# Performance work log

Hardware: AMD Instinct MI355X
Metric: run time of the kernel (lower is better)

## Reference

```python
import jax, jax.numpy as jnp
import numpy as np
import math

C_IN, C_OUT = 256, 256
KH, KW = 3, 3
STRIDE, PAD = 1, 1
CURV = 1.0
SQRT_C = math.sqrt(CURV)
EPS = 1e-15

def _beta(a, b):
    return math.exp(math.lgamma(a) + math.lgamma(b) - math.lgamma(a + b))

BETA_NI = _beta(C_IN / 2.0, 0.5)                 # beta(n_i/2, 1/2)
BETA_N = _beta(C_IN * KH * KW / 2.0, 0.5)        # beta(n/2, 1/2)


def logmap0(y, axis):
    n = jnp.maximum(jnp.linalg.norm(y, axis=axis, keepdims=True), EPS)
    return jnp.arctanh(jnp.minimum(SQRT_C * n, 1.0 - 1e-7)) * y / (SQRT_C * n)


def expmap0(v, axis):
    n = jnp.maximum(jnp.linalg.norm(v, axis=axis, keepdims=True), EPS)
    return jnp.tanh(SQRT_C * n) * v / (SQRT_C * n)


def unfold(x):
    # torch.nn.Unfold: x [B,C,H,W] -> [B, C*KH*KW, L], channel-major patch order
    B, C, H, W = x.shape
    Ho = (H + 2 * PAD - KH) // STRIDE + 1
    Wo = (W + 2 * PAD - KW) // STRIDE + 1
    xp = jnp.pad(x, ((0, 0), (0, 0), (PAD, PAD), (PAD, PAD)))
    cols = [xp[:, :, i:i + STRIDE * Ho:STRIDE, j:j + STRIDE * Wo:STRIDE]
            for i in range(KH) for j in range(KW)]
    patches = jnp.stack(cols, axis=2)            # [B, C, KH*KW, Ho, Wo]
    return patches.reshape(B, C * KH * KW, Ho * Wo), Ho, Wo


def poincare_fc(x, z, r):
    # x: [..., D_in] on ball, z: [D_in, D_out], r: [D_out]
    x2 = jnp.sum(x * x, axis=-1, keepdims=True)
    lam = 2.0 / (1.0 - CURV * x2)                # conformal factor lambda_x
    z_norm = jnp.maximum(jnp.linalg.norm(z, axis=0), EPS)  # [D_out]
    xz = x @ z                                   # [..., D_out]
    two_csr = 2.0 * SQRT_C * r
    inner = (SQRT_C * lam * xz / z_norm * jnp.cosh(two_csr)
             - (lam - 1.0) * jnp.sinh(two_csr))
    v = 2.0 * z_norm / SQRT_C * jnp.arcsinh(inner)   # hyperplane distances
    w = jnp.sinh(SQRT_C * v) / SQRT_C
    return w / (1.0 + jnp.sqrt(1.0 + CURV * jnp.sum(w * w, axis=-1, keepdims=True)))


def setup_inputs() -> dict:
    key = jax.random.key(0)
    k1, k2, k3 = jax.random.split(key, 3)
    # tangent vectors -> points on the Poincare ball (man_dim=1)
    v = 0.05 * jax.random.normal(k1, (16, C_IN, 64, 64), dtype=jnp.float32)
    x = expmap0(v, axis=1)
    std = (2.0 * C_IN * KH * KW * C_OUT) ** (-0.5)
    weights = std * jax.random.normal(k2, (KH * KW * C_IN, C_OUT), dtype=jnp.float32)
    bias = 0.01 * jax.random.normal(k3, (C_OUT,), dtype=jnp.float32)
    return {"x": x, "weights": weights, "bias": bias}


def reference(x, weights, bias):
    B = x.shape[0]
    v = logmap0(x, axis=1) * (BETA_N / BETA_NI)      # log map + beta scaling
    u, Ho, Wo = unfold(v)                            # [B, CK, L]
    u = jnp.swapaxes(u, 1, 2)                        # [B, L, CK]
    p = expmap0(u, axis=-1)                          # back onto the ball
    y = poincare_fc(p, weights, bias)                # [B, L, C_OUT]
    return jnp.swapaxes(y, 1, 2).reshape(B, C_OUT, Ho, Wo)
```

## Files before the change

### kernel.cpp

```cpp
#include <hip/hip_runtime.h>
#include <cmath>

typedef __bf16 bf16;
typedef __bf16 bf16x8 __attribute__((ext_vector_type(8)));
typedef float f32x4 __attribute__((ext_vector_type(4)));

#define SBAR() __builtin_amdgcn_sched_barrier(0)


__device__ inline void gload16(const void* g, void* l) {
    __builtin_amdgcn_global_load_lds(
        (const __attribute__((address_space(1))) unsigned int*)g,
        (__attribute__((address_space(3))) unsigned int*)l, 16, 0, 0);
}

__global__ void k_front(const float* __restrict__ x, const float* __restrict__ z,
                        const float* __restrict__ r, unsigned int* __restrict__ vt_u,
                        float* __restrict__ sq, bf16* __restrict__ zt5,
                        float* __restrict__ zn, float* __restrict__ ch,
                        float* __restrict__ sh, float Rbeta) {
    int blk = blockIdx.x;
    int tid = threadIdx.x;

    if (blk >= 2048) {
        int pb = blk - 2048;
        if (pb < 72) {
            int cc = pb / 9, tap = pb % 9;
            int co = tid;
#pragma unroll
            for (int g = 0; g < 4; ++g) {
                bf16x8 pk;
#pragma unroll
                for (int e = 0; e < 8; ++e) {
                    int c = cc * 32 + g * 8 + e;
                    pk[e] = (bf16)z[(size_t)(c * 9 + tap) * 256 + co];
                }
                *(bf16x8*)(zt5 + ((size_t)(pb * 4 + g) * 256 + co) * 8) = pk;
            }
        } else {
            __shared__ float redp[256];
            int co = pb - 72, t = tid;
            float s = 0.f;
            for (int i = 0; i < 9; ++i) {
                float v = z[(size_t)(i * 256 + t) * 256 + co];
                s += v * v;
            }
            redp[t] = s;
            __syncthreads();
            for (int off = 128; off >= 1; off >>= 1) {
                if (t < off) redp[t] += redp[t + off];
                __syncthreads();
            }
            if (t == 0) {
                zn[co] = fmaxf(sqrtf(redp[0]), 1e-15f);
                float tc = 2.f * r[co];
                ch[co] = coshf(tc);
                sh[co] = sinhf(tc);
            }
        }
        return;
    }

    __shared__ float tile[256][33];
    __shared__ float red[8][32];
    __shared__ float afac[32];
    int b = blk >> 7;
    int pix0 = (blk & 127) << 5;

    for (int it = 0; it < 8; ++it) {
        int c = it * 32 + (tid >> 3);
        int p4 = (tid & 7) * 4;
        f32x4 v = *(const f32x4*)(x + ((size_t)b * 256 + c) * 4096 + pix0 + p4);
        tile[c][p4] = v[0];
        tile[c][p4 + 1] = v[1];
        tile[c][p4 + 2] = v[2];
        tile[c][p4 + 3] = v[3];
    }
    __syncthreads();

    {
        int part = tid >> 5, p = tid & 31;
        float s = 0.f;
        for (int i = 0; i < 32; ++i) {
            float v = tile[part * 32 + i][p];
            s += v * v;
        }
        red[part][p] = s;
    }
    __syncthreads();
    if (tid < 32) {
        float n2 = 0.f;
        for (int i = 0; i < 8; ++i) n2 += red[i][tid];
        float n = sqrtf(n2);
        float nc = fmaxf(n, 1e-15f);
        float a = atanhf(fminf(nc, 0.9999999f)) / nc * Rbeta;
        afac[tid] = a;
        sq[(size_t)b * 4096 + pix0 + tid] = a * a * n2;
    }
    __syncthreads();

    for (int it = 0; it < 16; ++it) {
        int idx = it * 256 + tid;
        int p = idx >> 7;
        int cp = idx & 127;
        float a = afac[p];
        float v0 = a * tile[2 * cp][p];
        float v1 = a * tile[2 * cp + 1][p];
        union { bf16 h[2]; unsigned int u; } pk;
        pk.h[0] = (bf16)v0;
        pk.h[1] = (bf16)v1;
        vt_u[((size_t)b * 4096 + pix0 + p) * 128 + cp] = pk.u;
    }
}

__global__ void
__attribute__((amdgpu_flat_work_group_size(512, 512)))
__attribute__((amdgpu_waves_per_eu(4, 4)))
k_hconv(const bf16* __restrict__ vt, const bf16* __restrict__ zt5,
        const float* __restrict__ sq,
        const float* __restrict__ znp, const float* __restrict__ chp,
        const float* __restrict__ shp, float* __restrict__ out) {
    __shared__ __align__(1024) char Asb[16896];
    __shared__ __align__(1024) char Bsb[3][16448];
    __shared__ float s_lds[128], lam_lds[128];
    __shared__ float red[128][4];

    int tid = threadIdx.x;
    int bid = blockIdx.x;
    int bh = ((bid & 7) << 6) | (bid >> 3);
    int b = bh >> 5, h0 = (bh & 31) << 1;

    if (tid < 32) {
        int u = tid >> 1, side = tid & 1;
        *(f32x4*)(Asb + u * 1056 + side * 1040) = (f32x4){0.f, 0.f, 0.f, 0.f};
    }

    if (tid >= 128 && tid < 256) {
        int t = tid - 128;
        int h = h0 + (t >> 6), w = t & 63;
        const float* sb = sq + ((size_t)b << 12);
        float q = 0.f;
#pragma unroll
        for (int dh = -1; dh <= 1; ++dh) {
            int hhh = h + dh;
            if ((unsigned)hhh >= 64u) continue;
#pragma unroll
            for (int dw = -1; dw <= 1; ++dw) {
                int ww = w + dw;
                if ((unsigned)ww >= 64u) continue;
                q += sb[hhh * 64 + ww];
            }
        }
        float ncl = fmaxf(sqrtf(q), 1e-15f);
        float p = __expf(2.f * ncl);
        float tt = (p - 1.f) / (p + 1.f);
        s_lds[t] = tt / ncl;
        lam_lds[t] = 2.f / (1.f - tt * tt);
    }

    int wave = tid >> 6, lane = tid & 63;
    int wn = wave & 3, wm = wave >> 2;
    int lrow = lane & 15, lk = lane >> 4;

    f32x4 acc[4][4];
#pragma unroll
    for (int m = 0; m < 4; ++m)
#pragma unroll
        for (int n = 0; n < 4; ++n) acc[m][n] = (f32x4){0.f, 0.f, 0.f, 0.f};

    const bf16* vb = vt + (((size_t)b) << 12) * 256;

    auto stageA = [&](int ccn) {
#pragma unroll
        for (int it = 0; it < 2; ++it) {
            int u = wave * 2 + it;
            int r = u >> 2, g = u & 3;
            int hr = h0 - 1 + r;
            hr = hr < 0 ? 0 : (hr > 63 ? 63 : hr);
            const bf16* gp = vb + ((size_t)(hr * 64 + lane)) * 256 + ccn * 32 + g * 8;
            gload16(gp, Asb + u * 1056 + 16);
        }
    };
    auto stageB = [&](char* dst, int snext) {
        const char* src = (const char*)zt5 + (size_t)snext * 16384;
#pragma unroll
        for (int it = 0; it < 2; ++it) {
            int u = wave * 2 + it;
            gload16(src + u * 1024 + lane * 16,
                    dst + (u >> 2) * 4112 + (u & 3) * 1024);
        }
    };

    stageB((char*)Bsb[0], 0);
    stageA(0);
    __syncthreads();
    SBAR();

    const char* ApB = Asb + lk * 1056 + lrow * 16;
    const int bOff = lk * 4112 + wn * 1024 + lrow * 16;

#pragma unroll 1
    for (int cc = 0; cc < 8; ++cc) {
        const int sbase = cc * 9;
        const bool notlast = (cc < 7);

#pragma unroll
        for (int tap = 0; tap < 9; ++tap) {
            const int s = sbase + tap;
            const int dh = tap / 3 - 1, dw = tap % 3 - 1;
            const char* Ap = ApB + (wm + dh + 1) * 4224 + (dw + 1) * 16;

            bf16x8 a0, a1, a2, a3;
            if (tap != 0) {
                a0 = *(const bf16x8*)(Ap);
                a1 = *(const bf16x8*)(Ap + 256);
                a2 = *(const bf16x8*)(Ap + 512);
                a3 = *(const bf16x8*)(Ap + 768);
            }
            if (s < 71) stageB((char*)Bsb[(tap + 1) % 3], s + 1);
            SBAR();
            if (s < 71) { asm volatile("s_waitcnt vmcnt(2)" ::: "memory"); }
            else        { asm volatile("s_waitcnt vmcnt(0)" ::: "memory"); }
            SBAR();
            asm volatile("s_barrier" ::: "memory");
            SBAR();
            if (tap == 0) {
                a0 = *(const bf16x8*)(Ap);
                a1 = *(const bf16x8*)(Ap + 256);
                a2 = *(const bf16x8*)(Ap + 512);
                a3 = *(const bf16x8*)(Ap + 768);
            }

            int hh = h0 + wm + dh;
            if ((unsigned)hh < 64u) {
                const char* Bp = (const char*)Bsb[tap % 3] + bOff;
                bf16x8 b0 = *(const bf16x8*)(Bp);
                bf16x8 b1 = *(const bf16x8*)(Bp + 256);
                bf16x8 b2 = *(const bf16x8*)(Bp + 512);
                bf16x8 b3 = *(const bf16x8*)(Bp + 768);
                __builtin_amdgcn_s_setprio(1);
                acc[0][0] = __builtin_amdgcn_mfma_f32_16x16x32_bf16(a0, b0, acc[0][0], 0, 0, 0);
                acc[1][0] = __builtin_amdgcn_mfma_f32_16x16x32_bf16(a1, b0, acc[1][0], 0, 0, 0);
                acc[2][0] = __builtin_amdgcn_mfma_f32_16x16x32_bf16(a2, b0, acc[2][0], 0, 0, 0);
                acc[3][0] = __builtin_amdgcn_mfma_f32_16x16x32_bf16(a3, b0, acc[3][0], 0, 0, 0);
                acc[0][1] = __builtin_amdgcn_mfma_f32_16x16x32_bf16(a0, b1, acc[0][1], 0, 0, 0);
                acc[1][1] = __builtin_amdgcn_mfma_f32_16x16x32_bf16(a1, b1, acc[1][1], 0, 0, 0);
                acc[2][1] = __builtin_amdgcn_mfma_f32_16x16x32_bf16(a2, b1, acc[2][1], 0, 0, 0);
                acc[3][1] = __builtin_amdgcn_mfma_f32_16x16x32_bf16(a3, b1, acc[3][1], 0, 0, 0);
                acc[0][2] = __builtin_amdgcn_mfma_f32_16x16x32_bf16(a0, b2, acc[0][2], 0, 0, 0);
                acc[1][2] = __builtin_amdgcn_mfma_f32_16x16x32_bf16(a1, b2, acc[1][2], 0, 0, 0);
                acc[2][2] = __builtin_amdgcn_mfma_f32_16x16x32_bf16(a2, b2, acc[2][2], 0, 0, 0);
                acc[3][2] = __builtin_amdgcn_mfma_f32_16x16x32_bf16(a3, b2, acc[3][2], 0, 0, 0);
                acc[0][3] = __builtin_amdgcn_mfma_f32_16x16x32_bf16(a0, b3, acc[0][3], 0, 0, 0);
                acc[1][3] = __builtin_amdgcn_mfma_f32_16x16x32_bf16(a1, b3, acc[1][3], 0, 0, 0);
                acc[2][3] = __builtin_amdgcn_mfma_f32_16x16x32_bf16(a2, b3, acc[2][3], 0, 0, 0);
                acc[3][3] = __builtin_amdgcn_mfma_f32_16x16x32_bf16(a3, b3, acc[3][3], 0, 0, 0);
                __builtin_amdgcn_s_setprio(0);
            }
            SBAR();
            if (tap == 8) {
                asm volatile("s_barrier" ::: "memory");
                SBAR();
                if (notlast) stageA(cc + 1);
                SBAR();
            }
        }
    }

    float cz[4], sh4[4], tz[4];
#pragma unroll
    for (int n = 0; n < 4; ++n) {
        int co = wn * 64 + n * 16 + lrow;
        float zn = znp[co];
        cz[n] = chp[co] / zn;
        sh4[n] = shp[co];
        tz[n] = 2.f * zn;
    }

#pragma unroll
    for (int m = 0; m < 4; ++m) {
#pragma unroll
        for (int r = 0; r < 4; ++r) {
            int wp = wm * 64 + m * 16 + 4 * lk + r;
            float s = s_lds[wp], lam = lam_lds[wp];
            float lm1 = lam - 1.f;
            float psum = 0.f;
#pragma unroll
            for (int n = 0; n < 4; ++n) {
                float xz = s * acc[m][n][r];
                float inner = lam * xz * cz[n] - lm1 * sh4[n];
                float as = __logf(inner + sqrtf(inner * inner + 1.f));
                float p = __expf(tz[n] * as);
                float w = 0.5f * (p - __builtin_amdgcn_rcpf(p));
                acc[m][n][r] = w;
                psum += w * w;
            }
            psum += __shfl_xor(psum, 1);
            psum += __shfl_xor(psum, 2);
            psum += __shfl_xor(psum, 4);
            psum += __shfl_xor(psum, 8);
            if (lrow == 0) red[wp][wn] = psum;
        }
    }
    __syncthreads();

    float dinv[4][4];
#pragma unroll
    for (int m = 0; m < 4; ++m)
#pragma unroll
        for (int r = 0; r < 4; ++r) {
            int wp = wm * 64 + m * 16 + 4 * lk + r;
            float tot = (red[wp][0] + red[wp][1]) + (red[wp][2] + red[wp][3]);
            dinv[m][r] = __builtin_amdgcn_rcpf(1.f + sqrtf(1.f + tot));
        }

    float* ob = out + (size_t)b * 256 * 4096 + (h0 + wm) * 64;
#pragma unroll
    for (int m = 0; m < 4; ++m) {
#pragma unroll
        for (int n = 0; n < 4; ++n) {
            int co = wn * 64 + n * 16 + lrow;
            f32x4 o;
#pragma unroll
            for (int r = 0; r < 4; ++r) o[r] = acc[m][n][r] * dinv[m][r];
            *(f32x4*)(ob + (size_t)co * 4096 + m * 16 + 4 * lk) = o;
        }
    }
}

extern "C" void kernel_launch(void* const* d_in, const int* in_sizes, int n_in,
                              void* d_out, int out_size, void* d_ws, size_t ws_size,
                              hipStream_t stream) {
    const float* x = (const float*)d_in[0];
    const float* z = (const float*)d_in[1];
    const float* r = (const float*)d_in[2];
    float* out = (float*)d_out;

    char* ws = (char*)d_ws;
    bf16* vt = (bf16*)ws;
    float* sq = (float*)(ws + 33554432);
    bf16* zt5 = (bf16*)(ws + 34078720);
    float* zn = (float*)(ws + 35258368);
    float* ch = (float*)(ws + 35259392);
    float* sh = (float*)(ws + 35260416);
    if (ws_size < 35261440) return;

    double bni = lgamma(128.0) + lgamma(0.5) - lgamma(128.5);
    double bn = lgamma(1152.0) + lgamma(0.5) - lgamma(1152.5);
    float Rbeta = (float)exp(bn - bni);

    k_front<<<2376, 256, 0, stream>>>(x, z, r, (unsigned int*)vt, sq, zt5,
                                      zn, ch, sh, Rbeta);
    k_hconv<<<512, 512, 0, stream>>>(vt, zt5, sq, zn, ch, sh, out);
}
```

Measured before the change: 118.2 us.

## Switch implicit-GEMM conv inner loop to 32x32x16 bf16 MFMA tiles

Replaces the 4x4 grid of 16x16x32 MFMAs per wave with a 2x2 grid of 32x32x16 MFMAs, issued twice per tap to cover the K=32 chunk. LDS operand addressing for A and B fragments and the epilogue's output mapping, row reduction and stores are rewritten to match the 32x32 accumulator layout. The aim is fewer LDS fragment loads per MFMA and higher per-instruction throughput. The cost is a more complex epilogue with a wider shuffle reduction and a different store pattern, which may change bank conflicts.

```diff
diff --git a/kernel.cpp b/kernel.cpp
--- a/kernel.cpp
+++ b/kernel.cpp
@@ -4,6 +4,7 @@
 typedef __bf16 bf16;
 typedef __bf16 bf16x8 __attribute__((ext_vector_type(8)));
 typedef float f32x4 __attribute__((ext_vector_type(4)));
+typedef float f32x16 __attribute__((ext_vector_type(16)));
 
 #define SBAR() __builtin_amdgcn_sched_barrier(0)
 
@@ -160,13 +161,15 @@
 
     int wave = tid >> 6, lane = tid & 63;
     int wn = wave & 3, wm = wave >> 2;
-    int lrow = lane & 15, lk = lane >> 4;
-
-    f32x4 acc[4][4];
-#pragma unroll
-    for (int m = 0; m < 4; ++m)
-#pragma unroll
-        for (int n = 0; n < 4; ++n) acc[m][n] = (f32x4){0.f, 0.f, 0.f, 0.f};
+    int l31 = lane & 31, l5 = lane >> 5;
+
+    f32x16 acc[2][2];
+#pragma unroll
+    for (int m = 0; m < 2; ++m)
+#pragma unroll
+        for (int n = 0; n < 2; ++n)
+#pragma unroll
+            for (int e = 0; e < 16; ++e) acc[m][n][e] = 0.f;
 
     const bf16* vb = vt + (((size_t)b) << 12) * 256;
 
@@ -196,8 +199,8 @@
     __syncthreads();
     SBAR();
 
-    const char* ApB = Asb + lk * 1056 + lrow * 16;
-    const int bOff = lk * 4112 + wn * 1024 + lrow * 16;
+    const char* ApB = Asb + l5 * 1056 + (l31 + 1) * 16;
+    const int bOff = l5 * 4112 + (wn * 64 + l31) * 16;
 
 #pragma unroll 1
     for (int cc = 0; cc < 8; ++cc) {
@@ -208,14 +211,14 @@
         for (int tap = 0; tap < 9; ++tap) {
             const int s = sbase + tap;
             const int dh = tap / 3 - 1, dw = tap % 3 - 1;
-            const char* Ap = ApB + (wm + dh + 1) * 4224 + (dw + 1) * 16;
-
-            bf16x8 a0, a1, a2, a3;
+            const char* Ap = ApB + (wm + dh + 1) * 4224 + dw * 16;
+
+            bf16x8 a00, a10, a01, a11;
             if (tap != 0) {
-                a0 = *(const bf16x8*)(Ap);
-                a1 = *(const bf16x8*)(Ap + 256);
-                a2 = *(const bf16x8*)(Ap + 512);
-                a3 = *(const bf16x8*)(Ap + 768);
+                a00 = *(const bf16x8*)(Ap);
+                a10 = *(const bf16x8*)(Ap + 512);
+                a01 = *(const bf16x8*)(Ap + 2112);
+                a11 = *(const bf16x8*)(Ap + 2624);
             }
             if (s < 71) stageB((char*)Bsb[(tap + 1) % 3], s + 1);
             SBAR();
@@ -225,36 +228,28 @@
             asm volatile("s_barrier" ::: "memory");
             SBAR();
             if (tap == 0) {
-                a0 = *(const bf16x8*)(Ap);
-                a1 = *(const bf16x8*)(Ap + 256);
-                a2 = *(const bf16x8*)(Ap + 512);
-                a3 = *(const bf16x8*)(Ap + 768);
+                a00 = *(const bf16x8*)(Ap);
+                a10 = *(const bf16x8*)(Ap + 512);
+                a01 = *(const bf16x8*)(Ap + 2112);
+                a11 = *(const bf16x8*)(Ap + 2624);
             }
 
             int hh = h0 + wm + dh;
             if ((unsigned)hh < 64u) {
                 const char* Bp = (const char*)Bsb[tap % 3] + bOff;
-                bf16x8 b0 = *(const bf16x8*)(Bp);
-                bf16x8 b1 = *(const bf16x8*)(Bp + 256);
-                bf16x8 b2 = *(const bf16x8*)(Bp + 512);
-                bf16x8 b3 = *(const bf16x8*)(Bp + 768);
+                bf16x8 b00 = *(const bf16x8*)(Bp);
+                bf16x8 b10 = *(const bf16x8*)(Bp + 512);
+                bf16x8 b01 = *(const bf16x8*)(Bp + 8224);
+                bf16x8 b11 = *(const bf16x8*)(Bp + 8736);
                 __builtin_amdgcn_s_setprio(1);
-                acc[0][0] = __builtin_amdgcn_mfma_f32_16x16x32_bf16(a0, b0, acc[0][0], 0, 0, 0);
-                acc[1][0] = __builtin_amdgcn_mfma_f32_16x16x32_bf16(a1, b0, acc[1][0], 0, 0, 0);
-                acc[2][0] = __builtin_amdgcn_mfma_f32_16x16x32_bf16(a2, b0, acc[2][0], 0, 0, 0);
-                acc[3][0] = __builtin_amdgcn_mfma_f32_16x16x32_bf16(a3, b0, acc[3][0], 0, 0, 0);
-                acc[0][1] = __builtin_amdgcn_mfma_f32_16x16x32_bf16(a0, b1, acc[0][1], 0, 0, 0);
-                acc[1][1] = __builtin_amdgcn_mfma_f32_16x16x32_bf16(a1, b1, acc[1][1], 0, 0, 0);
-                acc[2][1] = __builtin_amdgcn_mfma_f32_16x16x32_bf16(a2, b1, acc[2][1], 0, 0, 0);
-                acc[3][1] = __builtin_amdgcn_mfma_f32_16x16x32_bf16(a3, b1, acc[3][1], 0, 0, 0);
-                acc[0][2] = __builtin_amdgcn_mfma_f32_16x16x32_bf16(a0, b2, acc[0][2], 0, 0, 0);
-                acc[1][2] = __builtin_amdgcn_mfma_f32_16x16x32_bf16(a1, b2, acc[1][2], 0, 0, 0);
-                acc[2][2] = __builtin_amdgcn_mfma_f32_16x16x32_bf16(a2, b2, acc[2][2], 0, 0, 0);
-                acc[3][2] = __builtin_amdgcn_mfma_f32_16x16x32_bf16(a3, b2, acc[3][2], 0, 0, 0);
-                acc[0][3] = __builtin_amdgcn_mfma_f32_16x16x32_bf16(a0, b3, acc[0][3], 0, 0, 0);
-                acc[1][3] = __builtin_amdgcn_mfma_f32_16x16x32_bf16(a1, b3, acc[1][3], 0, 0, 0);
-                acc[2][3] = __builtin_amdgcn_mfma_f32_16x16x32_bf16(a2, b3, acc[2][3], 0, 0, 0);
-                acc[3][3] = __builtin_amdgcn_mfma_f32_16x16x32_bf16(a3, b3, acc[3][3], 0, 0, 0);
+                acc[0][0] = __builtin_amdgcn_mfma_f32_32x32x16_bf16(a00, b00, acc[0][0], 0, 0, 0);
+                acc[1][0] = __builtin_amdgcn_mfma_f32_32x32x16_bf16(a10, b00, acc[1][0], 0, 0, 0);
+                acc[0][1] = __builtin_amdgcn_mfma_f32_32x32x16_bf16(a00, b10, acc[0][1], 0, 0, 0);
+                acc[1][1] = __builtin_amdgcn_mfma_f32_32x32x16_bf16(a10, b10, acc[1][1], 0, 0, 0);
+                acc[0][0] = __builtin_amdgcn_mfma_f32_32x32x16_bf16(a01, b01, acc[0][0], 0, 0, 0);
+                acc[1][0] = __builtin_amdgcn_mfma_f32_32x32x16_bf16(a11, b01, acc[1][0], 0, 0, 0);
+                acc[0][1] = __builtin_amdgcn_mfma_f32_32x32x16_bf16(a01, b11, acc[0][1], 0, 0, 0);
+                acc[1][1] = __builtin_amdgcn_mfma_f32_32x32x16_bf16(a11, b11, acc[1][1], 0, 0, 0);
                 __builtin_amdgcn_s_setprio(0);
             }
             SBAR();
@@ -267,63 +262,67 @@
         }
     }
 
-    float cz[4], sh4[4], tz[4];
-#pragma unroll
-    for (int n = 0; n < 4; ++n) {
-        int co = wn * 64 + n * 16 + lrow;
+    float cz[2], sh2[2], tz[2];
+#pragma unroll
+    for (int n = 0; n < 2; ++n) {
+        int co = wn * 64 + n * 32 + l31;
         float zn = znp[co];
         cz[n] = chp[co] / zn;
-        sh4[n] = shp[co];
+        sh2[n] = shp[co];
         tz[n] = 2.f * zn;
     }
 
 #pragma unroll
-    for (int m = 0; m < 4; ++m) {
-#pragma unroll
-        for (int r = 0; r < 4; ++r) {
-            int wp = wm * 64 + m * 16 + 4 * lk + r;
-            float s = s_lds[wp], lam = lam_lds[wp];
-            float lm1 = lam - 1.f;
-            float psum = 0.f;
-#pragma unroll
-            for (int n = 0; n < 4; ++n) {
-                float xz = s * acc[m][n][r];
-                float inner = lam * xz * cz[n] - lm1 * sh4[n];
-                float as = __logf(inner + sqrtf(inner * inner + 1.f));
-                float p = __expf(tz[n] * as);
-                float w = 0.5f * (p - __builtin_amdgcn_rcpf(p));
-                acc[m][n][r] = w;
-                psum += w * w;
-            }
-            psum += __shfl_xor(psum, 1);
-            psum += __shfl_xor(psum, 2);
-            psum += __shfl_xor(psum, 4);
-            psum += __shfl_xor(psum, 8);
-            if (lrow == 0) red[wp][wn] = psum;
-        }
-    }
-    __syncthreads();
-
-    float dinv[4][4];
-#pragma unroll
-    for (int m = 0; m < 4; ++m)
-#pragma unroll
-        for (int r = 0; r < 4; ++r) {
-            int wp = wm * 64 + m * 16 + 4 * lk + r;
-            float tot = (red[wp][0] + red[wp][1]) + (red[wp][2] + red[wp][3]);
-            dinv[m][r] = __builtin_amdgcn_rcpf(1.f + sqrtf(1.f + tot));
-        }
+    for (int m = 0; m < 2; ++m) {
+#pragma unroll
+        for (int q = 0; q < 4; ++q) {
+#pragma unroll
+            for (int j = 0; j < 4; ++j) {
+                int wp = wm * 64 + m * 32 + q * 8 + 4 * l5 + j;
+                float s = s_lds[wp], lam = lam_lds[wp];
+                float lm1 = lam - 1.f;
+                float psum = 0.f;
+#pragma unroll
+                for (int n = 0; n < 2; ++n) {
+                    float xz = s * acc[m][n][q * 4 + j];
+                    float inner = lam * xz * cz[n] - lm1 * sh2[n];
+                    float as = __logf(inner + sqrtf(inner * inner + 1.f));
+                    float p = __expf(tz[n] * as);
+                    float w = 0.5f * (p - __builtin_amdgcn_rcpf(p));
+                    acc[m][n][q * 4 + j] = w;
+                    psum += w * w;
+                }
+                psum += __shfl_xor(psum, 1);
+                psum += __shfl_xor(psum, 2);
+                psum += __shfl_xor(psum, 4);
+                psum += __shfl_xor(psum, 8);
+                psum += __shfl_xor(psum, 16);
+                if (l31 == 0) red[wp][wn] = psum;
+            }
+        }
+    }
+    __syncthreads();
 
     float* ob = out + (size_t)b * 256 * 4096 + (h0 + wm) * 64;
 #pragma unroll
-    for (int m = 0; m < 4; ++m) {
-#pragma unroll
-        for (int n = 0; n < 4; ++n) {
-            int co = wn * 64 + n * 16 + lrow;
-            f32x4 o;
-#pragma unroll
-            for (int r = 0; r < 4; ++r) o[r] = acc[m][n][r] * dinv[m][r];
-            *(f32x4*)(ob + (size_t)co * 4096 + m * 16 + 4 * lk) = o;
+    for (int m = 0; m < 2; ++m) {
+#pragma unroll
+        for (int q = 0; q < 4; ++q) {
+            f32x4 dv;
+#pragma unroll
+            for (int j = 0; j < 4; ++j) {
+                int wp = wm * 64 + m * 32 + q * 8 + 4 * l5 + j;
+                float tot = (red[wp][0] + red[wp][1]) + (red[wp][2] + red[wp][3]);
+                dv[j] = __builtin_amdgcn_rcpf(1.f + sqrtf(1.f + tot));
+            }
+#pragma unroll
+            for (int n = 0; n < 2; ++n) {
+                int co = wn * 64 + n * 32 + l31;
+                f32x4 o;
+#pragma unroll
+                for (int j = 0; j < 4; ++j) o[j] = acc[m][n][q * 4 + j] * dv[j];
+                *(f32x4*)(ob + (size_t)co * 4096 + m * 32 + q * 8 + 4 * l5) = o;
+            }
         }
     }
 }
```

Result: slower. 122.6 us (+3.8%).
